# Kernel tuning notes

Hardware: AMD Instinct MI355X
Metric: run time of the kernel (lower is better)

## Reference

```python
import jax, jax.numpy as jnp
import numpy as np

B, NK, HID, EMB, KEY, VOCAB = 64, 2048, 1024, 512, 512, 50257


def setup_inputs() -> dict:
    key = jax.random.key(0)
    ks = jax.random.split(key, 14)
    s = 0.02
    return {
        "input_ids": jax.random.randint(ks[0], (1, B, 1), 0, VOCAB),
        "hidden": jax.random.normal(ks[1], (1, B, HID), jnp.float32),
        "annotations": jax.random.normal(ks[2], (B, NK, KEY), jnp.float32),
        # embedding table
        "emb_table": jax.random.normal(ks[3], (VOCAB, EMB), jnp.float32) * s,
        # additive (Bahdanau) attention params: score = v . tanh(K Wk + Q Wq + b)
        "Wk": jax.random.normal(ks[4], (KEY, HID), jnp.float32) * s,
        "Wq": jax.random.normal(ks[5], (HID, HID), jnp.float32) * s,
        "bk": jnp.zeros((HID,), jnp.float32),
        "v_attn": jax.random.normal(ks[6], (HID,), jnp.float32) * s,
        # GRU (single layer, single step): input size EMB+KEY, hidden HID
        "W_ih": jax.random.normal(ks[7], (3 * HID, EMB + KEY), jnp.float32) * s,
        "W_hh": jax.random.normal(ks[8], (3 * HID, HID), jnp.float32) * s,
        "b_ih": jnp.zeros((3 * HID,), jnp.float32),
        "b_hh": jnp.zeros((3 * HID,), jnp.float32),
        # output projection to vocab
        "W_out": jax.random.normal(ks[9], (VOCAB, HID), jnp.float32) * s,
        "b_out": jnp.zeros((VOCAB,), jnp.float32),
    }


def reference(input_ids, hidden, annotations, emb_table, Wk, Wq, bk, v_attn,
              W_ih, W_hh, b_ih, b_hh, W_out, b_out):
    # embedding(input).squeeze(2): [1,B,1] -> [1,B,EMB]; dropout is eval-mode identity
    emb = emb_table[input_ids[:, :, 0]]
    Q = hidden[0]                                                   # [B,HID]
    # additive attention over annotations (K = V = annotations)
    feat = jnp.tanh(annotations @ Wk + (Q @ Wq)[:, None, :] + bk)    # [B,NK,HID]
    scores = jnp.einsum('bnh,h->bn', feat, v_attn)                   # [B,NK]
    a = jax.nn.softmax(scores, axis=-1)
    context = jnp.einsum('bn,bnk->bk', a, annotations)               # [B,KEY]
    # single-step GRU on concat(emb, context)
    x = jnp.concatenate([emb[0], context], axis=1)                   # [B,EMB+KEY]
    gi = x @ W_ih.T + b_ih
    gh = Q @ W_hh.T + b_hh
    ir, iz, inn = jnp.split(gi, 3, axis=1)
    hr, hz, hn = jnp.split(gh, 3, axis=1)
    r = jax.nn.sigmoid(ir + hr)
    z = jax.nn.sigmoid(iz + hz)
    n = jnp.tanh(inn + r * hn)
    h_new = (1.0 - z) * n + z * Q                                    # [B,HID]
    o = h_new[None]                                                  # [1,B,HID]
    logits = o @ W_out.T + b_out                                     # [1,B,VOCAB]
    logp = jax.nn.log_softmax(logits, axis=2)
    return logp, o, a
```

## Files before the change

kernel.cpp:

```cpp
#include <hip/hip_runtime.h>
#include <hip/hip_bf16.h>
#include <cstddef>

#define BATCH 64
#define NK    2048
#define HID   1024
#define EMB   512
#define KEY   512
#define VOCAB 50257

typedef __attribute__((ext_vector_type(8))) short bf16x8;
typedef __attribute__((ext_vector_type(4))) short bf16x4;
typedef __attribute__((ext_vector_type(4))) float f32x4;

__device__ __forceinline__ short f2bf(float f) {
    unsigned u = __builtin_bit_cast(unsigned, f);
    unsigned r = (u + 0x7FFFu + ((u >> 16) & 1u)) >> 16;
    return (short)r;
}

#define GLOAD_LDS16(g, l)                                                  \
    __builtin_amdgcn_global_load_lds(                                      \
        (const __attribute__((address_space(1))) void*)(g),                \
        (__attribute__((address_space(3))) void*)(l), 16, 0, 0)

__global__ void wkt_kernel(const float* __restrict__ Wk, short* __restrict__ wkT) {
    __shared__ float t[32][33];
    int k0 = blockIdx.x << 5, n0 = blockIdx.y << 5;
    int tx = threadIdx.x, ty = threadIdx.y;
#pragma unroll
    for (int i = 0; i < 4; ++i)
        t[ty + i * 8][tx] = Wk[(size_t)(k0 + ty + i * 8) * 1024 + n0 + tx];
    __syncthreads();
#pragma unroll
    for (int i = 0; i < 4; ++i)
        wkT[(size_t)(n0 + ty + i * 8) * 512 + k0 + tx] = f2bf(t[tx][ty + i * 8]);
}

template <int TB>
__global__ __launch_bounds__(256) void sgemm64(const float* __restrict__ A,
                                               const float* __restrict__ B,
                                               float* __restrict__ C, int N, int K) {
    __shared__ float As2[32][68];
    __shared__ float Bs2[32][68];
    int tid = threadIdx.x;
    int n0 = blockIdx.x << 6;
    int kb = blockIdx.y << 7;
    int tn = (tid & 15) << 2, tm = (tid >> 4) << 2;
    float acc[4][4] = {};
    for (int kc = 0; kc < 128; kc += 32) {
        int kk = kb + kc;
#pragma unroll
        for (int i = 0; i < 8; ++i) {
            int idx = i * 256 + tid;
            int ml = idx >> 5, kl = idx & 31;
            As2[kl][ml] = A[(size_t)ml * K + kk + kl];
        }
        if (TB) {
#pragma unroll
            for (int i = 0; i < 8; ++i) {
                int idx = i * 256 + tid;
                int nl = idx >> 5, kl = idx & 31;
                Bs2[kl][nl] = B[(size_t)(n0 + nl) * K + kk + kl];
            }
        } else {
#pragma unroll
            for (int i = 0; i < 8; ++i) {
                int idx = i * 256 + tid;
                int kl = idx >> 6, nl = idx & 63;
                Bs2[kl][nl] = B[(size_t)(kk + kl) * N + n0 + nl];
            }
        }
        __syncthreads();
#pragma unroll
        for (int k = 0; k < 32; ++k) {
            float a0 = As2[k][tm], a1 = As2[k][tm + 1], a2 = As2[k][tm + 2], a3 = As2[k][tm + 3];
            float b0 = Bs2[k][tn], b1 = Bs2[k][tn + 1], b2 = Bs2[k][tn + 2], b3 = Bs2[k][tn + 3];
            acc[0][0] += a0 * b0; acc[0][1] += a0 * b1; acc[0][2] += a0 * b2; acc[0][3] += a0 * b3;
            acc[1][0] += a1 * b0; acc[1][1] += a1 * b1; acc[1][2] += a1 * b2; acc[1][3] += a1 * b3;
            acc[2][0] += a2 * b0; acc[2][1] += a2 * b1; acc[2][2] += a2 * b2; acc[2][3] += a2 * b3;
            acc[3][0] += a3 * b0; acc[3][1] += a3 * b1; acc[3][2] += a3 * b2; acc[3][3] += a3 * b3;
        }
        __syncthreads();
    }
#pragma unroll
    for (int i = 0; i < 4; ++i)
#pragma unroll
        for (int j = 0; j < 4; ++j)
            atomicAdd(&C[(size_t)(tm + i) * N + n0 + tn + j], acc[i][j]);
}

__global__ __launch_bounds__(512, 4) void scores_kernel(const float* __restrict__ ann,
                                                        const short* __restrict__ wkT,
                                                        const float* __restrict__ qc,
                                                        const float* __restrict__ bk,
                                                        const float* __restrict__ vat,
                                                        float* __restrict__ scores2) {
    __shared__ __align__(16) short As[128 * 32];
    __shared__ __align__(16) short Bs[256 * 32];
    __shared__ float red[128][4];

    int bx = blockIdx.x;
    int rb = ((bx >> 4) << 3) | (bx & 7);
    int hs = (bx >> 3) & 1;
    int row0 = rb << 7;
    int b = row0 >> 11;
    int tid = threadIdx.x, lane = tid & 63, wv = tid >> 6;
    int wm = wv & 1, wn = wv >> 1;
    int q = lane >> 4, c = lane & 15;

    int sm = tid >> 2;
    int sq = tid & 3;
    int sxor = (tid >> 3) & 3;
    int aphys = sq ^ sxor;
    int bqlog = sq ^ sxor;
    int swz = (q ^ ((c >> 1) & 3)) << 3;

    const float* qcb = qc + b * 1024;
    float pscore[4][4] = {};

    for (int nc = 0; nc < 2; ++nc) {
        f32x4 acc[4][4];
#pragma unroll
        for (int mi = 0; mi < 4; ++mi)
#pragma unroll
            for (int ni = 0; ni < 4; ++ni)
                acc[mi][ni] = (f32x4){0.f, 0.f, 0.f, 0.f};

        int nbase = hs * 512 + nc * 256;
        for (int ks = 0; ks < 16; ++ks) {
            int k0 = ks << 5;
            __syncthreads();
            const float* asrc = ann + (size_t)(row0 + sm) * 512 + k0 + sq * 8;
            float4 a0 = *(const float4*)asrc;
            float4 a1 = *(const float4*)(asrc + 4);
            bf16x8 ap;
            ap[0] = f2bf(a0.x); ap[1] = f2bf(a0.y); ap[2] = f2bf(a0.z); ap[3] = f2bf(a0.w);
            ap[4] = f2bf(a1.x); ap[5] = f2bf(a1.y); ap[6] = f2bf(a1.z); ap[7] = f2bf(a1.w);
            *(bf16x8*)(As + sm * 32 + aphys * 8) = ap;
            {
                const short* b0 = wkT + (size_t)(nbase + sm) * 512 + k0 + bqlog * 8;
                const short* b1 = b0 + 128 * 512;
                GLOAD_LDS16(b0, Bs + (wv << 9));
                GLOAD_LDS16(b1, Bs + 4096 + (wv << 9));
            }
            __syncthreads();
            bf16x8 af[4];
#pragma unroll
            for (int mi = 0; mi < 4; ++mi)
                af[mi] = *(const bf16x8*)(As + (wm * 64 + mi * 16 + c) * 32 + swz);
#pragma unroll
            for (int ni = 0; ni < 4; ++ni) {
                bf16x8 bfr = *(const bf16x8*)(Bs + (wn * 64 + ni * 16 + c) * 32 + swz);
#pragma unroll
                for (int mi = 0; mi < 4; ++mi)
                    acc[mi][ni] = __builtin_amdgcn_mfma_f32_16x16x32_bf16(af[mi], bfr, acc[mi][ni], 0, 0, 0);
            }
        }
        int hbase = nbase + wn * 64;
#pragma unroll
        for (int ni = 0; ni < 4; ++ni) {
            int h = hbase + ni * 16 + c;
            float qv = qcb[h] + bk[h];
            float vv = vat[h];
#pragma unroll
            for (int mi = 0; mi < 4; ++mi)
#pragma unroll
                for (int rg = 0; rg < 4; ++rg) {
                    float xv = acc[mi][ni][rg] + qv;
                    float e = __expf(2.0f * xv);
                    pscore[mi][rg] += (1.0f - 2.0f / (e + 1.0f)) * vv;
                }
        }
    }

#pragma unroll
    for (int mi = 0; mi < 4; ++mi)
#pragma unroll
        for (int rg = 0; rg < 4; ++rg) {
            float p = pscore[mi][rg];
            p += __shfl_xor(p, 1, 16);
            p += __shfl_xor(p, 2, 16);
            p += __shfl_xor(p, 4, 16);
            p += __shfl_xor(p, 8, 16);
            if (c == 0) red[wm * 64 + mi * 16 + q * 4 + rg][wn] = p;
        }
    __syncthreads();
    if (tid < 128)
        scores2[(size_t)hs * 131072 + row0 + tid] =
            red[tid][0] + red[tid][1] + red[tid][2] + red[tid][3];
}

__global__ __launch_bounds__(256) void softmax_kernel(const float* __restrict__ scores2,
                                                      float* __restrict__ a_out) {
    __shared__ float red[4];
    int b = blockIdx.x, tid = threadIdx.x;
    const float* s0 = scores2 + b * 2048;
    const float* s1 = s0 + 131072;
    float loc[8];
    float vmax = -1e30f;
#pragma unroll
    for (int i = 0; i < 8; ++i) {
        loc[i] = s0[tid + i * 256] + s1[tid + i * 256];
        vmax = fmaxf(vmax, loc[i]);
    }
#pragma unroll
    for (int m = 32; m; m >>= 1) vmax = fmaxf(vmax, __shfl_xor(vmax, m));
    if ((tid & 63) == 0) red[tid >> 6] = vmax;
    __syncthreads();
    vmax = fmaxf(fmaxf(red[0], red[1]), fmaxf(red[2], red[3]));
    float sum = 0.f;
#pragma unroll
    for (int i = 0; i < 8; ++i) { loc[i] = __expf(loc[i] - vmax); sum += loc[i]; }
#pragma unroll
    for (int m = 32; m; m >>= 1) sum += __shfl_xor(sum, m);
    __syncthreads();
    if ((tid & 63) == 0) red[tid >> 6] = sum;
    __syncthreads();
    sum = red[0] + red[1] + red[2] + red[3];
    float inv = 1.0f / sum;
#pragma unroll
    for (int i = 0; i < 8; ++i) a_out[b * 2048 + tid + i * 256] = loc[i] * inv;
}

__global__ __launch_bounds__(256) void context_kernel(const float* __restrict__ a_out,
                                                      const float* __restrict__ ann,
                                                      float* __restrict__ ctxpart) {
    int b = blockIdx.y, nch = blockIdx.x, n0 = nch << 7;
    int k = threadIdx.x << 1;
    const float* base = ann + ((size_t)b * 2048 + n0) * 512 + k;
    const float* av = a_out + b * 2048 + n0;
    float ax = 0.f, ay = 0.f;
    for (int n = 0; n < 128; ++n) {
        float w = av[n];
        float2 v = *(const float2*)(base + (size_t)n * 512);
        ax += w * v.x;
        ay += w * v.y;
    }
    float* dst = ctxpart + ((size_t)nch * 64 + b) * 512 + k;
    dst[0] = ax;
    dst[1] = ay;
}

__global__ void x_kernel(const int* __restrict__ ids, const float* __restrict__ emb,
                         const float* __restrict__ ctxpart, float* __restrict__ x) {
    int idx = blockIdx.x * 256 + threadIdx.x;
    int b = idx >> 10, k = idx & 1023;
    if (k < 512) {
        x[idx] = emb[(size_t)ids[b] * 512 + k];
    } else {
        int kk = k - 512;
        float s = 0.f;
#pragma unroll
        for (int i = 0; i < 16; ++i) s += ctxpart[((size_t)i * 64 + b) * 512 + kk];
        x[idx] = s;
    }
}

__global__ void gru_kernel(const float* __restrict__ gi, const float* __restrict__ gh,
                           const float* __restrict__ bih, const float* __restrict__ bhh,
                           const float* __restrict__ hidden, float* __restrict__ o_out,
                           short* __restrict__ hbf) {
    int idx = blockIdx.x * 256 + threadIdx.x;
    int b = idx >> 10, h = idx & 1023;
    const float* gib = gi + b * 3072;
    const float* ghb = gh + b * 3072;
    float ir = gib[h] + bih[h],               hr = ghb[h] + bhh[h];
    float iz = gib[1024 + h] + bih[1024 + h], hz = ghb[1024 + h] + bhh[1024 + h];
    float in = gib[2048 + h] + bih[2048 + h], hn = ghb[2048 + h] + bhh[2048 + h];
    float r = 1.0f / (1.0f + __expf(-(ir + hr)));
    float z = 1.0f / (1.0f + __expf(-(iz + hz)));
    float nn = tanhf(in + r * hn);
    float hq = hidden[idx];
    float hnew = (1.0f - z) * nn + z * hq;
    o_out[idx] = hnew;
    hbf[idx] = f2bf(hnew);
}

__global__ __launch_bounds__(256) void logits_kernel(const short* __restrict__ hbf,
                                                     const float* __restrict__ Wout,
                                                     const float* __restrict__ bout,
                                                     float* __restrict__ logits) {
    int tid = threadIdx.x, lane = tid & 63, wv = tid >> 6;
    int q = lane >> 4, c = lane & 15;
    int v = blockIdx.x * 64 + wv * 16 + c;
    int vc = v < VOCAB ? v : (VOCAB - 1);
    const float* wrow = Wout + (size_t)vc * 1024;
    f32x4 acc[4];
#pragma unroll
    for (int mi = 0; mi < 4; ++mi) acc[mi] = (f32x4){0.f, 0.f, 0.f, 0.f};
#pragma unroll 4
    for (int ks = 0; ks < 32; ++ks) {
        int k0 = ks * 32 + q * 8;
        float4 w0 = *(const float4*)(wrow + k0);
        float4 w1 = *(const float4*)(wrow + k0 + 4);
        bf16x8 bfr;
        bfr[0] = f2bf(w0.x); bfr[1] = f2bf(w0.y); bfr[2] = f2bf(w0.z); bfr[3] = f2bf(w0.w);
        bfr[4] = f2bf(w1.x); bfr[5] = f2bf(w1.y); bfr[6] = f2bf(w1.z); bfr[7] = f2bf(w1.w);
#pragma unroll
        for (int mi = 0; mi < 4; ++mi) {
            bf16x8 af = *(const bf16x8*)(hbf + (size_t)(mi * 16 + c) * 1024 + k0);
            acc[mi] = __builtin_amdgcn_mfma_f32_16x16x32_bf16(af, bfr, acc[mi], 0, 0, 0);
        }
    }
    if (v < VOCAB) {
        float bo = bout[v];
#pragma unroll
        for (int mi = 0; mi < 4; ++mi)
#pragma unroll
            for (int rg = 0; rg < 4; ++rg) {
                int row = mi * 16 + q * 4 + rg;
                logits[(size_t)row * VOCAB + v] = acc[mi][rg] + bo;
            }
    }
}

__global__ __launch_bounds__(1024) void logsoftmax_kernel(float* __restrict__ logp) {
    __shared__ float red[16];
    int b = blockIdx.x, tid = threadIdx.x;
    float* row = logp + (size_t)b * VOCAB;
    float vmax = -1e30f;
    for (int i = tid; i < VOCAB; i += 1024) vmax = fmaxf(vmax, row[i]);
#pragma unroll
    for (int m = 32; m; m >>= 1) vmax = fmaxf(vmax, __shfl_xor(vmax, m));
    if ((tid & 63) == 0) red[tid >> 6] = vmax;
    __syncthreads();
    float m0 = red[0];
#pragma unroll
    for (int i = 1; i < 16; ++i) m0 = fmaxf(m0, red[i]);
    vmax = m0;
    float sum = 0.f;
    for (int i = tid; i < VOCAB; i += 1024) sum += __expf(row[i] - vmax);
#pragma unroll
    for (int m = 32; m; m >>= 1) sum += __shfl_xor(sum, m);
    __syncthreads();
    if ((tid & 63) == 0) red[tid >> 6] = sum;
    __syncthreads();
    float s0 = 0.f;
#pragma unroll
    for (int i = 0; i < 16; ++i) s0 += red[i];
    float lse = vmax + logf(s0);
    for (int i = tid; i < VOCAB; i += 1024) row[i] = row[i] - lse;
}

extern "C" void kernel_launch(void* const* d_in, const int* in_sizes, int n_in,
                              void* d_out, int out_size, void* d_ws, size_t ws_size,
                              hipStream_t stream) {
    const int* ids      = (const int*)d_in[0];
    const float* hidden = (const float*)d_in[1];
    const float* ann    = (const float*)d_in[2];
    const float* embT   = (const float*)d_in[3];
    const float* Wk     = (const float*)d_in[4];
    const float* Wq     = (const float*)d_in[5];
    const float* bk     = (const float*)d_in[6];
    const float* vat    = (const float*)d_in[7];
    const float* Wih    = (const float*)d_in[8];
    const float* Whh    = (const float*)d_in[9];
    const float* bih    = (const float*)d_in[10];
    const float* bhh    = (const float*)d_in[11];
    const float* Wout   = (const float*)d_in[12];
    const float* bout   = (const float*)d_in[13];

    float* out   = (float*)d_out;
    float* logp  = out;
    float* o_out = out + (size_t)BATCH * VOCAB;
    float* a_out = o_out + BATCH * HID;

    float* shared0 = (float*)d_ws;
    float* scores2 = shared0;
    float* ctxpart = shared0;
    float* qc      = shared0 + 524288;
    float* gh      = qc + 65536;
    float* gi      = gh + 196608;
    float* x       = gi + 196608;
    short* wkT     = (short*)(x + 65536);
    short* hbf     = wkT + 524288;

    hipMemsetAsync(qc, 0, (size_t)458752 * sizeof(float), stream);

    wkt_kernel<<<dim3(16, 32), dim3(32, 8), 0, stream>>>(Wk, wkT);
    sgemm64<0><<<dim3(16, 8), 256, 0, stream>>>(hidden, Wq, qc, 1024, 1024);
    sgemm64<1><<<dim3(48, 8), 256, 0, stream>>>(hidden, Whh, gh, 3072, 1024);
    scores_kernel<<<2048, 512, 0, stream>>>(ann, wkT, qc, bk, vat, scores2);
    softmax_kernel<<<64, 256, 0, stream>>>(scores2, a_out);
    context_kernel<<<dim3(16, 64), 256, 0, stream>>>(a_out, ann, ctxpart);
    x_kernel<<<256, 256, 0, stream>>>(ids, embT, ctxpart, x);
    sgemm64<1><<<dim3(48, 8), 256, 0, stream>>>(x, Wih, gi, 3072, 1024);
    gru_kernel<<<256, 256, 0, stream>>>(gi, gh, bih, bhh, hidden, o_out, hbf);
    logits_kernel<<<(VOCAB + 63) / 64, 256, 0, stream>>>(hbf, Wout, bout, logp);
    logsoftmax_kernel<<<64, 1024, 0, stream>>>(logp);
}
```

Measured before the change: 1.017 ms.

## Double-buffer LDS tiles in scores kernel to overlap loads with MFMA

Rewrites the scores GEMM main loop to double-buffer the A and B LDS tiles and flattens the two N chunks into one 32-step loop. The next step's tiles are staged while MFMAs run on the current buffer, and annotations are register-prefetched two steps ahead. This halves the barriers per step and aims to hide global-load latency, at the cost of doubled LDS use (which may reduce occupancy) and extra live registers.

Measured after the change: 908.8 us. 10.6% less time.

```diff
diff --git a/kernel.cpp b/kernel.cpp
--- a/kernel.cpp
+++ b/kernel.cpp
@@ -96,8 +96,8 @@
                                                         const float* __restrict__ bk,
                                                         const float* __restrict__ vat,
                                                         float* __restrict__ scores2) {
-    __shared__ __align__(16) short As[128 * 32];
-    __shared__ __align__(16) short Bs[256 * 32];
+    __shared__ __align__(16) short As[2 * 128 * 32];
+    __shared__ __align__(16) short Bs[2 * 256 * 32];
     __shared__ float red[128][4];
 
     int bx = blockIdx.x;
@@ -117,61 +117,83 @@
     int swz = (q ^ ((c >> 1) & 3)) << 3;
 
     const float* qcb = qc + b * 1024;
+    const float* abase = ann + (size_t)(row0 + sm) * 512 + sq * 8;
+    const short* bbase = wkT + (size_t)(hs * 512 + sm) * 512 + bqlog * 8;
+
     float pscore[4][4] = {};
-
-    for (int nc = 0; nc < 2; ++nc) {
-        f32x4 acc[4][4];
+    f32x4 acc[4][4];
+#pragma unroll
+    for (int mi = 0; mi < 4; ++mi)
+#pragma unroll
+        for (int ni = 0; ni < 4; ++ni)
+            acc[mi][ni] = (f32x4){0.f, 0.f, 0.f, 0.f};
+
+    float4 pa0 = *(const float4*)abase;
+    float4 pa1 = *(const float4*)(abase + 4);
+    GLOAD_LDS16(bbase, Bs + (wv << 9));
+    GLOAD_LDS16(bbase + 128 * 512, Bs + 4096 + (wv << 9));
+    {
+        bf16x8 ap;
+        ap[0] = f2bf(pa0.x); ap[1] = f2bf(pa0.y); ap[2] = f2bf(pa0.z); ap[3] = f2bf(pa0.w);
+        ap[4] = f2bf(pa1.x); ap[5] = f2bf(pa1.y); ap[6] = f2bf(pa1.z); ap[7] = f2bf(pa1.w);
+        *(bf16x8*)(As + sm * 32 + aphys * 8) = ap;
+    }
+    pa0 = *(const float4*)(abase + 32);
+    pa1 = *(const float4*)(abase + 36);
+    __syncthreads();
+
+#pragma unroll 2
+    for (int t = 0; t < 32; ++t) {
+        short* Asc = As + (t & 1) * 4096;
+        short* Bsc = Bs + ((t & 1) << 13);
+        short* Asn = As + ((t & 1) ^ 1) * 4096;
+        short* Bsn = Bs + (((t & 1) ^ 1) << 13);
+        if (t < 31) {
+            int t1 = t + 1;
+            const short* bs = bbase + (size_t)((t1 >> 4) * (256 * 512)) + ((t1 & 15) << 5);
+            GLOAD_LDS16(bs, Bsn + (wv << 9));
+            GLOAD_LDS16(bs + 128 * 512, Bsn + 4096 + (wv << 9));
+            bf16x8 ap;
+            ap[0] = f2bf(pa0.x); ap[1] = f2bf(pa0.y); ap[2] = f2bf(pa0.z); ap[3] = f2bf(pa0.w);
+            ap[4] = f2bf(pa1.x); ap[5] = f2bf(pa1.y); ap[6] = f2bf(pa1.z); ap[7] = f2bf(pa1.w);
+            *(bf16x8*)(Asn + sm * 32 + aphys * 8) = ap;
+        }
+        if (t < 30) {
+            const float* as = abase + (((t + 2) & 15) << 5);
+            pa0 = *(const float4*)as;
+            pa1 = *(const float4*)(as + 4);
+        }
+        bf16x8 af[4];
 #pragma unroll
         for (int mi = 0; mi < 4; ++mi)
-#pragma unroll
-            for (int ni = 0; ni < 4; ++ni)
-                acc[mi][ni] = (f32x4){0.f, 0.f, 0.f, 0.f};
-
-        int nbase = hs * 512 + nc * 256;
-        for (int ks = 0; ks < 16; ++ks) {
-            int k0 = ks << 5;
-            __syncthreads();
-            const float* asrc = ann + (size_t)(row0 + sm) * 512 + k0 + sq * 8;
-            float4 a0 = *(const float4*)asrc;
-            float4 a1 = *(const float4*)(asrc + 4);
-            bf16x8 ap;
-            ap[0] = f2bf(a0.x); ap[1] = f2bf(a0.y); ap[2] = f2bf(a0.z); ap[3] = f2bf(a0.w);
-            ap[4] = f2bf(a1.x); ap[5] = f2bf(a1.y); ap[6] = f2bf(a1.z); ap[7] = f2bf(a1.w);
-            *(bf16x8*)(As + sm * 32 + aphys * 8) = ap;
-            {
-                const short* b0 = wkT + (size_t)(nbase + sm) * 512 + k0 + bqlog * 8;
-                const short* b1 = b0 + 128 * 512;
-                GLOAD_LDS16(b0, Bs + (wv << 9));
-                GLOAD_LDS16(b1, Bs + 4096 + (wv << 9));
+            af[mi] = *(const bf16x8*)(Asc + (wm * 64 + mi * 16 + c) * 32 + swz);
+#pragma unroll
+        for (int ni = 0; ni < 4; ++ni) {
+            bf16x8 bfr = *(const bf16x8*)(Bsc + (wn * 64 + ni * 16 + c) * 32 + swz);
+#pragma unroll
+            for (int mi = 0; mi < 4; ++mi)
+                acc[mi][ni] = __builtin_amdgcn_mfma_f32_16x16x32_bf16(af[mi], bfr, acc[mi][ni], 0, 0, 0);
+        }
+        if ((t & 15) == 15) {
+            int hbase = hs * 512 + (t >> 4) * 256 + wn * 64;
+#pragma unroll
+            for (int ni = 0; ni < 4; ++ni) {
+                int h = hbase + ni * 16 + c;
+                float qv = qcb[h] + bk[h];
+                float vv = vat[h];
+#pragma unroll
+                for (int mi = 0; mi < 4; ++mi) {
+#pragma unroll
+                    for (int rg = 0; rg < 4; ++rg) {
+                        float xv = acc[mi][ni][rg] + qv;
+                        float e = __expf(2.0f * xv);
+                        pscore[mi][rg] += (1.0f - 2.0f / (e + 1.0f)) * vv;
+                        acc[mi][ni][rg] = 0.f;
+                    }
+                }
             }
-            __syncthreads();
-            bf16x8 af[4];
-#pragma unroll
-            for (int mi = 0; mi < 4; ++mi)
-                af[mi] = *(const bf16x8*)(As + (wm * 64 + mi * 16 + c) * 32 + swz);
-#pragma unroll
-            for (int ni = 0; ni < 4; ++ni) {
-                bf16x8 bfr = *(const bf16x8*)(Bs + (wn * 64 + ni * 16 + c) * 32 + swz);
-#pragma unroll
-                for (int mi = 0; mi < 4; ++mi)
-                    acc[mi][ni] = __builtin_amdgcn_mfma_f32_16x16x32_bf16(af[mi], bfr, acc[mi][ni], 0, 0, 0);
-            }
-        }
-        int hbase = nbase + wn * 64;
-#pragma unroll
-        for (int ni = 0; ni < 4; ++ni) {
-            int h = hbase + ni * 16 + c;
-            float qv = qcb[h] + bk[h];
-            float vv = vat[h];
-#pragma unroll
-            for (int mi = 0; mi < 4; ++mi)
-#pragma unroll
-                for (int rg = 0; rg < 4; ++rg) {
-                    float xv = acc[mi][ni][rg] + qv;
-                    float e = __expf(2.0f * xv);
-                    pscore[mi][rg] += (1.0f - 2.0f / (e + 1.0f)) * vv;
-                }
-        }
+        }
+        __syncthreads();
     }
 
 #pragma unroll
```
